# Kernel tuning notes

Hardware: AMD Instinct MI355X
Metric: run time of the kernel (lower is better)

Reference implementation:

```python
import jax, jax.numpy as jnp
import numpy as np

N = 50000       # nodes
E = 800000      # edges (avg degree 16)
D = 64          # input_dim
G = 512         # graphs in batch
HID = 64        # hidden_dim


def setup_inputs() -> dict:
    key = jax.random.key(0)
    ks = jax.random.split(key, 8)
    x = jax.random.normal(ks[0], (N, D), dtype=jnp.float32)
    edge_index = jax.random.randint(ks[1], (2, E), 0, N, dtype=jnp.int64)
    batch = jnp.sort(jax.random.randint(ks[2], (N,), 0, G, dtype=jnp.int64))
    # glorot-ish scaled weights
    W1 = jax.random.normal(ks[3], (D, D), dtype=jnp.float32) * (1.0 / np.sqrt(D))
    b1 = jnp.zeros((D,), dtype=jnp.float32)
    W2 = jax.random.normal(ks[4], (D, 2 * D), dtype=jnp.float32) * (1.0 / np.sqrt(D))
    b2 = jnp.zeros((2 * D,), dtype=jnp.float32)
    Wfc = jax.random.normal(ks[5], (2 * D, HID), dtype=jnp.float32) * (1.0 / np.sqrt(2 * D))
    bfc = jnp.zeros((HID,), dtype=jnp.float32)
    return {"x": x, "edge_index": edge_index, "batch": batch,
            "W1": W1, "b1": b1, "W2": W2, "b2": b2, "Wfc": Wfc, "bfc": bfc}


def _gcn_edges(edge_index, n):
    # add self-loops (PyG GCNConv default) and symmetric normalization
    loop = jnp.arange(n, dtype=edge_index.dtype)
    src = jnp.concatenate([edge_index[0], loop])
    dst = jnp.concatenate([edge_index[1], loop])
    deg = jnp.zeros((n,), jnp.float32).at[dst].add(1.0)  # in-degree incl. self-loop
    dinv = jax.lax.rsqrt(deg)                            # deg >= 1 always
    norm = dinv[src] * dinv[dst]                         # [E+N]
    return src, dst, norm


def _gcn_conv(x, src, dst, norm, W, b):
    h = x @ W                                   # transform first (N, out)
    msg = h[src] * norm[:, None]                # gather + scale (E+N, out)
    out = jnp.zeros_like(h).at[dst].add(msg)    # scatter-add at destination
    return out + b


def reference(x, edge_index, batch, W1, b1, W2, b2, Wfc, bfc):
    n = x.shape[0]
    src, dst, norm = _gcn_edges(edge_index, n)
    h = jax.nn.relu(_gcn_conv(x, src, dst, norm, W1, b1))   # [N, D]
    h = _gcn_conv(h, src, dst, norm, W2, b2)                # [N, 2D]
    # global mean pool per graph
    sums = jax.ops.segment_sum(h, batch, num_segments=G)    # [G, 2D]
    cnt = jax.ops.segment_sum(jnp.ones((n,), h.dtype), batch, num_segments=G)
    pooled = sums / jnp.maximum(cnt, 1.0)[:, None]
    # dropout is identity in eval mode
    return pooled @ Wfc + bfc                                # [G, HID]
```

## Files before the change

kernel.cpp:

```cpp
#include <hip/hip_runtime.h>
#include <hip/hip_fp16.h>

#define NN 50000
#define EE 800000
#define DD 64
#define GG 512
#define HIDD 64
#define D2 128
#define NBLK 196

__device__ inline __half2 mk2(float a, float b) {
    __half2 h; h.x = __float2half_rn(a); h.y = __float2half_rn(b); return h;
}

__global__ void k_zero(int* __restrict__ cnt_in, int* __restrict__ part) {
    int i = blockIdx.x * blockDim.x + threadIdx.x;
    if (i < NN) cnt_in[i] = 0;
    if (i < 256) part[i] = 0;
}

__global__ void k_count_rank(const int* __restrict__ dst, int* __restrict__ cnt_in,
                             int* __restrict__ rank) {
    int e = blockIdx.x * blockDim.x + threadIdx.x;
    if (e < EE) rank[e] = atomicAdd(&cnt_in[dst[e]], 1);
}

__global__ void k_partial(const int* __restrict__ cnt_in, int* __restrict__ part) {
    __shared__ int s[256];
    int t = threadIdx.x, i = blockIdx.x * 256 + t;
    s[t] = (i < NN) ? cnt_in[i] : 0;
    __syncthreads();
    for (int off = 128; off > 0; off >>= 1) {
        if (t < off) s[t] += s[t + off];
        __syncthreads();
    }
    if (t == 0) part[blockIdx.x] = s[0];
}

__global__ void k_scanp(int* __restrict__ part) {
    __shared__ int s[256];
    int t = threadIdx.x;
    int v = part[t];
    s[t] = v;
    __syncthreads();
    for (int off = 1; off < 256; off <<= 1) {
        int add = (t >= off) ? s[t - off] : 0;
        __syncthreads();
        s[t] += add;
        __syncthreads();
    }
    part[t] = s[t] - v;
}

__global__ void k_rowptr(const int* __restrict__ cnt_in, const int* __restrict__ part,
                         int* __restrict__ rowptr) {
    __shared__ int s[256];
    int t = threadIdx.x, i = blockIdx.x * 256 + t;
    int v = (i < NN) ? cnt_in[i] : 0;
    s[t] = v;
    __syncthreads();
    for (int off = 1; off < 256; off <<= 1) {
        int add = (t >= off) ? s[t - off] : 0;
        __syncthreads();
        s[t] += add;
        __syncthreads();
    }
    int excl = s[t] - v + part[blockIdx.x];
    if (i <= NN) rowptr[i] = excl;
}

__global__ void k_place(const int* __restrict__ src, const int* __restrict__ dst,
                        const int* __restrict__ rank, const int* __restrict__ rowptr,
                        int* __restrict__ csr) {
    int e = blockIdx.x * blockDim.x + threadIdx.x;
    if (e < EE)
        csr[rowptr[dst[e]] + rank[e]] = src[e];
}

__global__ __launch_bounds__(256) void k_gemm1(const float* __restrict__ x,
        const float* __restrict__ W1, const int* __restrict__ cnt_in,
        __half2* __restrict__ t1h) {
    __shared__ float As[128][68];
    __shared__ float Bs[DD][DD];
    int t = threadIdx.x;
    int row0 = blockIdx.x * 128;
    #pragma unroll
    for (int j = 0; j < 4; ++j) {
        int id = t + j * 256;
        int k = id >> 4, c4 = (id & 15) * 4;
        *(float4*)&Bs[k][c4] = *(const float4*)&W1[k * DD + c4];
    }
    #pragma unroll
    for (int j = 0; j < 8; ++j) {
        int id = t + j * 256;
        int r = id >> 4, k4 = (id & 15) * 4;
        int gr = row0 + r;
        float4 v = make_float4(0.f, 0.f, 0.f, 0.f);
        if (gr < NN) v = *(const float4*)&x[gr * DD + k4];
        *(float4*)&As[r][k4] = v;
    }
    __syncthreads();
    int rbase = (t >> 3) * 4, cbase = (t & 7) * 8;
    float4 cL0 = make_float4(0.f,0.f,0.f,0.f), cH0 = cL0;
    float4 cL1 = cL0, cH1 = cL0, cL2 = cL0, cH2 = cL0, cL3 = cL0, cH3 = cL0;
    #pragma unroll 2
    for (int k = 0; k < DD; ++k) {
        float4 bL = *(const float4*)&Bs[k][cbase];
        float4 bH = *(const float4*)&Bs[k][cbase + 4];
        float a0 = As[rbase + 0][k];
        float a1 = As[rbase + 1][k];
        float a2 = As[rbase + 2][k];
        float a3 = As[rbase + 3][k];
        cL0 += bL * a0;  cH0 += bH * a0;
        cL1 += bL * a1;  cH1 += bH * a1;
        cL2 += bL * a2;  cH2 += bH * a2;
        cL3 += bL * a3;  cH3 += bH * a3;
    }
    int h2base = (t & 7) * 4;
    int gr0 = row0 + rbase;
    #define STORE_T1(idx, CL, CH) \
        if (gr0 + idx < NN) { \
            float d = rsqrtf((float)cnt_in[gr0 + idx] + 1.0f); \
            __half2 p0 = mk2(CL.x * d, CL.y * d), p1 = mk2(CL.z * d, CL.w * d); \
            __half2 p2 = mk2(CH.x * d, CH.y * d), p3 = mk2(CH.z * d, CH.w * d); \
            uint4 pk; pk.x = *(unsigned*)&p0; pk.y = *(unsigned*)&p1; \
            pk.z = *(unsigned*)&p2; pk.w = *(unsigned*)&p3; \
            *(uint4*)(t1h + (size_t)(gr0 + idx) * 32 + h2base) = pk; }
    STORE_T1(0, cL0, cH0)
    STORE_T1(1, cL1, cH1)
    STORE_T1(2, cL2, cH2)
    STORE_T1(3, cL3, cH3)
    #undef STORE_T1
}

__global__ __launch_bounds__(256) void k_agg1(const int* __restrict__ rowptr,
        const int* __restrict__ csr, const __half2* __restrict__ t1h,
        const int* __restrict__ cnt_in, const float* __restrict__ b1,
        __half2* __restrict__ u_h) {
    int gid = blockIdx.x * blockDim.x + threadIdx.x;
    int node = gid >> 5;
    int p = threadIdx.x & 31;
    if (node >= NN) return;
    int beg = rowptr[node], end = rowptr[node + 1];
    float2 A0 = __half22float2(t1h[(size_t)node * 32 + p]);
    float2 A1 = make_float2(0.f, 0.f), A2 = A1, A3 = A1;
    int e = beg;
    for (; e + 4 <= end; e += 4) {
        int s0 = csr[e], s1 = csr[e + 1], s2 = csr[e + 2], s3 = csr[e + 3];
        float2 v0 = __half22float2(t1h[(size_t)s0 * 32 + p]);
        float2 v1 = __half22float2(t1h[(size_t)s1 * 32 + p]);
        float2 v2 = __half22float2(t1h[(size_t)s2 * 32 + p]);
        float2 v3 = __half22float2(t1h[(size_t)s3 * 32 + p]);
        A0.x += v0.x; A0.y += v0.y;
        A1.x += v1.x; A1.y += v1.y;
        A2.x += v2.x; A2.y += v2.y;
        A3.x += v3.x; A3.y += v3.y;
    }
    for (; e < end; ++e) {
        float2 v = __half22float2(t1h[(size_t)csr[e] * 32 + p]);
        A0.x += v.x; A0.y += v.y;
    }
    float sx = (A0.x + A1.x) + (A2.x + A3.x);
    float sy = (A0.y + A1.y) + (A2.y + A3.y);
    float d = rsqrtf((float)cnt_in[node] + 1.0f);
    float2 bb = ((const float2*)b1)[p];
    float h0 = fmaxf(d * sx + bb.x, 0.0f);
    float h1 = fmaxf(d * sy + bb.y, 0.0f);
    u_h[(size_t)node * 32 + p] = mk2(d * h0, d * h1);
}

__global__ __launch_bounds__(256) void k_agg2(const int* __restrict__ rowptr,
        const int* __restrict__ csr, const __half2* __restrict__ u_h,
        const int* __restrict__ cnt_in, float* __restrict__ w) {
    int gid = blockIdx.x * blockDim.x + threadIdx.x;
    int node = gid >> 5;
    int p = threadIdx.x & 31;
    if (node >= NN) return;
    int beg = rowptr[node], end = rowptr[node + 1];
    float2 A0 = __half22float2(u_h[(size_t)node * 32 + p]);
    float2 A1 = make_float2(0.f, 0.f), A2 = A1, A3 = A1;
    int e = beg;
    for (; e + 4 <= end; e += 4) {
        int s0 = csr[e], s1 = csr[e + 1], s2 = csr[e + 2], s3 = csr[e + 3];
        float2 v0 = __half22float2(u_h[(size_t)s0 * 32 + p]);
        float2 v1 = __half22float2(u_h[(size_t)s1 * 32 + p]);
        float2 v2 = __half22float2(u_h[(size_t)s2 * 32 + p]);
        float2 v3 = __half22float2(u_h[(size_t)s3 * 32 + p]);
        A0.x += v0.x; A0.y += v0.y;
        A1.x += v1.x; A1.y += v1.y;
        A2.x += v2.x; A2.y += v2.y;
        A3.x += v3.x; A3.y += v3.y;
    }
    for (; e < end; ++e) {
        float2 v = __half22float2(u_h[(size_t)csr[e] * 32 + p]);
        A0.x += v.x; A0.y += v.y;
    }
    float d = rsqrtf((float)cnt_in[node] + 1.0f);
    float sx = (A0.x + A1.x) + (A2.x + A3.x);
    float sy = (A0.y + A1.y) + (A2.y + A3.y);
    ((float2*)&w[(size_t)node * DD])[p] = make_float2(d * sx, d * sy);
}

__global__ __launch_bounds__(256) void k_gemm2(const float* __restrict__ w,
        const float* __restrict__ W2, const float* __restrict__ b2,
        float* __restrict__ acc2) {
    __shared__ float As[DD][68];
    __shared__ float Bs[DD][D2];
    int t = threadIdx.x;
    int row0 = blockIdx.x * 64;
    #pragma unroll
    for (int j = 0; j < 8; ++j) {
        int id = t + j * 256;
        int k = id >> 5, c4 = (id & 31) * 4;
        *(float4*)&Bs[k][c4] = *(const float4*)&W2[k * D2 + c4];
    }
    #pragma unroll
    for (int j = 0; j < 4; ++j) {
        int id = t + j * 256;
        int r = id >> 4, k4 = (id & 15) * 4;
        int gr = row0 + r;
        float4 v = make_float4(0.f, 0.f, 0.f, 0.f);
        if (gr < NN) v = *(const float4*)&w[gr * DD + k4];
        *(float4*)&As[r][k4] = v;
    }
    __syncthreads();
    int rbase = (t >> 4) * 4, cbase = (t & 15) * 8;
    float4 cL0 = make_float4(0.f,0.f,0.f,0.f), cH0 = cL0;
    float4 cL1 = cL0, cH1 = cL0, cL2 = cL0, cH2 = cL0, cL3 = cL0, cH3 = cL0;
    #pragma unroll 2
    for (int k = 0; k < DD; ++k) {
        float4 bL = *(const float4*)&Bs[k][cbase];
        float4 bH = *(const float4*)&Bs[k][cbase + 4];
        float a0 = As[rbase + 0][k];
        float a1 = As[rbase + 1][k];
        float a2 = As[rbase + 2][k];
        float a3 = As[rbase + 3][k];
        cL0 += bL * a0;  cH0 += bH * a0;
        cL1 += bL * a1;  cH1 += bH * a1;
        cL2 += bL * a2;  cH2 += bH * a2;
        cL3 += bL * a3;  cH3 += bH * a3;
    }
    float4 b2L = *(const float4*)&b2[cbase];
    float4 b2H = *(const float4*)&b2[cbase + 4];
    int gr0 = row0 + rbase;
    if (gr0 + 0 < NN) {
        *(float4*)&acc2[(gr0 + 0) * D2 + cbase] = cL0 + b2L;
        *(float4*)&acc2[(gr0 + 0) * D2 + cbase + 4] = cH0 + b2H; }
    if (gr0 + 1 < NN) {
        *(float4*)&acc2[(gr0 + 1) * D2 + cbase] = cL1 + b2L;
        *(float4*)&acc2[(gr0 + 1) * D2 + cbase + 4] = cH1 + b2H; }
    if (gr0 + 2 < NN) {
        *(float4*)&acc2[(gr0 + 2) * D2 + cbase] = cL2 + b2L;
        *(float4*)&acc2[(gr0 + 2) * D2 + cbase + 4] = cH2 + b2H; }
    if (gr0 + 3 < NN) {
        *(float4*)&acc2[(gr0 + 3) * D2 + cbase] = cL3 + b2L;
        *(float4*)&acc2[(gr0 + 3) * D2 + cbase + 4] = cH3 + b2H; }
}

__global__ __launch_bounds__(128) void k_pool2(const float* __restrict__ acc2,
        const int* __restrict__ batch, const float* __restrict__ Wfc,
        const float* __restrict__ bfc, float* __restrict__ out) {
    int g = blockIdx.x;
    int t = threadIdx.x;
    int lo = 0, hi = NN;
    while (lo < hi) { int mid = (lo + hi) >> 1; if (batch[mid] < g) lo = mid + 1; else hi = mid; }
    int beg = lo;
    hi = NN;
    while (lo < hi) { int mid = (lo + hi) >> 1; if (batch[mid] < g + 1) lo = mid + 1; else hi = mid; }
    int end = lo;

    float s0 = 0.0f, s1 = 0.0f;
    int i = beg;
    for (; i + 2 <= end; i += 2) {
        s0 += acc2[i * D2 + t];
        s1 += acc2[(i + 1) * D2 + t];
    }
    if (i < end) s0 += acc2[i * D2 + t];

    int n = end - beg;
    float pooledv = (n > 0) ? ((s0 + s1) / (float)n) : 0.0f;

    __shared__ float pm[D2];
    pm[t] = pooledv;
    __syncthreads();
    if (t < HIDD) {
        float o = bfc[t];
        #pragma unroll
        for (int k = 0; k < D2; ++k)
            o += pm[k] * Wfc[k * HIDD + t];
        out[g * HIDD + t] = o;
    }
}

extern "C" void kernel_launch(void* const* d_in, const int* in_sizes, int n_in,
                              void* d_out, int out_size, void* d_ws, size_t ws_size,
                              hipStream_t stream) {
    const float* x     = (const float*)d_in[0];
    const int*   ei    = (const int*)  d_in[1];
    const int*   batch = (const int*)  d_in[2];
    const float* W1    = (const float*)d_in[3];
    const float* b1    = (const float*)d_in[4];
    const float* W2    = (const float*)d_in[5];
    const float* b2    = (const float*)d_in[6];
    const float* Wfc   = (const float*)d_in[7];
    const float* bfc   = (const float*)d_in[8];
    float* out = (float*)d_out;

    const int* src = ei;
    const int* dst = ei + EE;

    char* base = (char*)d_ws;
    __half2* t1h  = (__half2*)base;
    __half2* u_h  = (__half2*)(base + (size_t)NN * 128);
    float*   acc2 = (float*)base;
    float*   w    = (float*)(base + (size_t)NN * 512);
    int* iws    = (int*)(base + (size_t)NN * 512 + (size_t)NN * 256);
    int* cnt_in = iws;
    int* rowptr = cnt_in + 50048;
    int* part   = rowptr + 50304;
    int* rank   = part + 256;
    int* csr    = rank + EE;

    k_zero      <<<NBLK, 256, 0, stream>>>(cnt_in, part);
    k_count_rank<<<(EE + 255) / 256, 256, 0, stream>>>(dst, cnt_in, rank);
    k_partial   <<<NBLK, 256, 0, stream>>>(cnt_in, part);
    k_scanp     <<<1, 256, 0, stream>>>(part);
    k_rowptr    <<<NBLK, 256, 0, stream>>>(cnt_in, part, rowptr);
    k_place     <<<(EE + 255) / 256, 256, 0, stream>>>(src, dst, rank, rowptr, csr);
    k_gemm1     <<<(NN + 127) / 128, 256, 0, stream>>>(x, W1, cnt_in, t1h);
    k_agg1      <<<(NN * 32 + 255) / 256, 256, 0, stream>>>(rowptr, csr, t1h, cnt_in, b1, u_h);
    k_agg2      <<<(NN * 32 + 255) / 256, 256, 0, stream>>>(rowptr, csr, u_h, cnt_in, w);
    k_gemm2     <<<(NN + 63) / 64, 256, 0, stream>>>(w, W2, b2, acc2);
    k_pool2     <<<GG, 128, 0, stream>>>(acc2, batch, Wfc, bfc, out);
}
```

Measured before the change: 237.0 us.

## Pool before second GEMM using linearity, drop per-node W2 transform

Uses linearity of mean pooling to average the aggregated 64-wide features per graph first, then apply W2 and b2 once per graph instead of once per node. This removes the N x 64 x 128 GEMM kernel and the 128-wide intermediate write and read. Bias is added only for non-empty graphs so the result matches the reference. The per-graph block now does a small 64x128 matvec, and the sum order changes slightly.

```diff
diff --git a/kernel.cpp b/kernel.cpp
--- a/kernel.cpp
+++ b/kernel.cpp
@@ -201,93 +201,48 @@
     ((float2*)&w[(size_t)node * DD])[p] = make_float2(d * sx, d * sy);
 }
 
-__global__ __launch_bounds__(256) void k_gemm2(const float* __restrict__ w,
-        const float* __restrict__ W2, const float* __restrict__ b2,
-        float* __restrict__ acc2) {
-    __shared__ float As[DD][68];
-    __shared__ float Bs[DD][D2];
-    int t = threadIdx.x;
-    int row0 = blockIdx.x * 64;
-    #pragma unroll
-    for (int j = 0; j < 8; ++j) {
-        int id = t + j * 256;
-        int k = id >> 5, c4 = (id & 31) * 4;
-        *(float4*)&Bs[k][c4] = *(const float4*)&W2[k * D2 + c4];
-    }
-    #pragma unroll
-    for (int j = 0; j < 4; ++j) {
-        int id = t + j * 256;
-        int r = id >> 4, k4 = (id & 15) * 4;
-        int gr = row0 + r;
-        float4 v = make_float4(0.f, 0.f, 0.f, 0.f);
-        if (gr < NN) v = *(const float4*)&w[gr * DD + k4];
-        *(float4*)&As[r][k4] = v;
-    }
-    __syncthreads();
-    int rbase = (t >> 4) * 4, cbase = (t & 15) * 8;
-    float4 cL0 = make_float4(0.f,0.f,0.f,0.f), cH0 = cL0;
-    float4 cL1 = cL0, cH1 = cL0, cL2 = cL0, cH2 = cL0, cL3 = cL0, cH3 = cL0;
-    #pragma unroll 2
-    for (int k = 0; k < DD; ++k) {
-        float4 bL = *(const float4*)&Bs[k][cbase];
-        float4 bH = *(const float4*)&Bs[k][cbase + 4];
-        float a0 = As[rbase + 0][k];
-        float a1 = As[rbase + 1][k];
-        float a2 = As[rbase + 2][k];
-        float a3 = As[rbase + 3][k];
-        cL0 += bL * a0;  cH0 += bH * a0;
-        cL1 += bL * a1;  cH1 += bH * a1;
-        cL2 += bL * a2;  cH2 += bH * a2;
-        cL3 += bL * a3;  cH3 += bH * a3;
-    }
-    float4 b2L = *(const float4*)&b2[cbase];
-    float4 b2H = *(const float4*)&b2[cbase + 4];
-    int gr0 = row0 + rbase;
-    if (gr0 + 0 < NN) {
-        *(float4*)&acc2[(gr0 + 0) * D2 + cbase] = cL0 + b2L;
-        *(float4*)&acc2[(gr0 + 0) * D2 + cbase + 4] = cH0 + b2H; }
-    if (gr0 + 1 < NN) {
-        *(float4*)&acc2[(gr0 + 1) * D2 + cbase] = cL1 + b2L;
-        *(float4*)&acc2[(gr0 + 1) * D2 + cbase + 4] = cH1 + b2H; }
-    if (gr0 + 2 < NN) {
-        *(float4*)&acc2[(gr0 + 2) * D2 + cbase] = cL2 + b2L;
-        *(float4*)&acc2[(gr0 + 2) * D2 + cbase + 4] = cH2 + b2H; }
-    if (gr0 + 3 < NN) {
-        *(float4*)&acc2[(gr0 + 3) * D2 + cbase] = cL3 + b2L;
-        *(float4*)&acc2[(gr0 + 3) * D2 + cbase + 4] = cH3 + b2H; }
-}
-
-__global__ __launch_bounds__(128) void k_pool2(const float* __restrict__ acc2,
-        const int* __restrict__ batch, const float* __restrict__ Wfc,
+__global__ __launch_bounds__(128) void k_pool2(const float* __restrict__ w,
+        const int* __restrict__ batch, const float* __restrict__ W2,
+        const float* __restrict__ b2, const float* __restrict__ Wfc,
         const float* __restrict__ bfc, float* __restrict__ out) {
     int g = blockIdx.x;
     int t = threadIdx.x;
+    int c = t & 63, half = t >> 6;
     int lo = 0, hi = NN;
     while (lo < hi) { int mid = (lo + hi) >> 1; if (batch[mid] < g) lo = mid + 1; else hi = mid; }
     int beg = lo;
     hi = NN;
     while (lo < hi) { int mid = (lo + hi) >> 1; if (batch[mid] < g + 1) lo = mid + 1; else hi = mid; }
     int end = lo;
-
-    float s0 = 0.0f, s1 = 0.0f;
-    int i = beg;
-    for (; i + 2 <= end; i += 2) {
-        s0 += acc2[i * D2 + t];
-        s1 += acc2[(i + 1) * D2 + t];
-    }
-    if (i < end) s0 += acc2[i * D2 + t];
-
     int n = end - beg;
-    float pooledv = (n > 0) ? ((s0 + s1) / (float)n) : 0.0f;
-
-    __shared__ float pm[D2];
-    pm[t] = pooledv;
+
+    float s = 0.0f;
+    for (int i = beg + half; i < end; i += 2)
+        s += w[(size_t)i * DD + c];
+
+    __shared__ float sm[128];
+    __shared__ float pm[DD];
+    __shared__ float tt[D2];
+    sm[t] = s;
+    __syncthreads();
+    if (t < DD) {
+        float scale = (n > 0) ? (1.0f / (float)n) : 0.0f;
+        pm[t] = (sm[t] + sm[t + 64]) * scale;
+    }
+    __syncthreads();
+    {
+        float acc = (n > 0) ? b2[t] : 0.0f;
+        #pragma unroll 4
+        for (int k = 0; k < DD; ++k)
+            acc += pm[k] * W2[k * D2 + t];
+        tt[t] = acc;
+    }
     __syncthreads();
     if (t < HIDD) {
         float o = bfc[t];
-        #pragma unroll
+        #pragma unroll 4
         for (int k = 0; k < D2; ++k)
-            o += pm[k] * Wfc[k * HIDD + t];
+            o += tt[k] * Wfc[k * HIDD + t];
         out[g * HIDD + t] = o;
     }
 }
@@ -312,7 +267,6 @@
     char* base = (char*)d_ws;
     __half2* t1h  = (__half2*)base;
     __half2* u_h  = (__half2*)(base + (size_t)NN * 128);
-    float*   acc2 = (float*)base;
     float*   w    = (float*)(base + (size_t)NN * 512);
     int* iws    = (int*)(base + (size_t)NN * 512 + (size_t)NN * 256);
     int* cnt_in = iws;
@@ -330,6 +284,5 @@
     k_gemm1     <<<(NN + 127) / 128, 256, 0, stream>>>(x, W1, cnt_in, t1h);
     k_agg1      <<<(NN * 32 + 255) / 256, 256, 0, stream>>>(rowptr, csr, t1h, cnt_in, b1, u_h);
     k_agg2      <<<(NN * 32 + 255) / 256, 256, 0, stream>>>(rowptr, csr, u_h, cnt_in, w);
-    k_gemm2     <<<(NN + 63) / 64, 256, 0, stream>>>(w, W2, b2, acc2);
-    k_pool2     <<<GG, 128, 0, stream>>>(acc2, batch, Wfc, bfc, out);
-}
+    k_pool2     <<<GG, 128, 0, stream>>>(w, batch, W2, b2, Wfc, bfc, out);
+}
```

After: 219.8 us. 7.3% less time.
